# Kernel optimization log

Hardware: AMD Instinct MI355X
Metric: run time of the kernel (lower is better)

## Reference

```python
import jax, jax.numpy as jnp
import numpy as np

N = 8192
IN_DIM = 512
MEM_DIM = 512


def _linear_params(k, fan_in, fan_out):
    kw, kb = jax.random.split(k)
    s = 1.0 / np.sqrt(fan_in)
    W = jax.random.uniform(kw, (fan_in, fan_out), jnp.float32, -s, s)
    b = jax.random.uniform(kb, (fan_out,), jnp.float32, -s, s)
    return W, b


def setup_inputs() -> dict:
    key = jax.random.key(0)
    ks = jax.random.split(key, 12)
    inputs = jax.random.normal(ks[0], (N, IN_DIM), jnp.float32)
    # tree.type is a [1,2] mixing matrix per node (lang vs vis weights)
    type_mask = jax.nn.softmax(jax.random.normal(ks[1], (N, 2), jnp.float32), axis=-1)
    # topologically ordered tree: parent slot of node i is in [0, i]; slot 0 = virtual zero root state
    rng = np.random.default_rng(0)
    parent = np.zeros(N, dtype=np.int32)
    for i in range(1, N):
        parent[i] = rng.integers(0, i + 1)
    d = {"inputs": inputs, "type_mask": type_mask, "parent": jnp.asarray(parent)}
    names = ["ioux_vis", "iouh_vis", "fx_vis", "fh_vis",
             "ioux_lang", "iouh_lang", "fx_lang", "fh_lang"]
    fanins = [IN_DIM, MEM_DIM, IN_DIM, MEM_DIM] * 2
    fanouts = [3 * MEM_DIM, 3 * MEM_DIM, MEM_DIM, MEM_DIM] * 2
    for j, nm in enumerate(names):
        W, b = _linear_params(ks[2 + j], fanins[j], fanouts[j])
        d["W_" + nm] = W
        d["b_" + nm] = b
    return d


def reference(inputs, type_mask, parent,
              W_ioux_vis, b_ioux_vis, W_iouh_vis, b_iouh_vis,
              W_fx_vis, b_fx_vis, W_fh_vis, b_fh_vis,
              W_ioux_lang, b_ioux_lang, W_iouh_lang, b_iouh_lang,
              W_fx_lang, b_fx_lang, W_fh_lang, b_fh_lang):
    n_nodes = inputs.shape[0]
    D = W_fh_vis.shape[1]
    # batch the input-dependent projections into big GEMMs (fused across all nodes)
    x_iou_v = inputs @ W_ioux_vis + b_ioux_vis  # [N, 3D]
    x_f_v = inputs @ W_fx_vis + b_fx_vis        # [N, D]
    x_iou_l = inputs @ W_ioux_lang + b_ioux_lang
    x_f_l = inputs @ W_fx_lang + b_fx_lang

    def node(x_iou, x_f, h_p, c_p, W_iouh, b_iouh, W_fh, b_fh):
        iou = x_iou + h_p @ W_iouh + b_iouh  # [3D]
        i, o, u = jnp.split(iou, 3)
        f = jax.nn.sigmoid(x_f + h_p @ W_fh + b_fh)
        c = jax.nn.sigmoid(i) * jnp.tanh(u) + f * c_p
        h = jax.nn.sigmoid(o) * jnp.tanh(c)
        return c, h

    # slot 0 holds the zero state used by root nodes; node i lives at slot i+1
    c0 = jnp.zeros((n_nodes + 1, D), inputs.dtype)
    h0 = jnp.zeros((n_nodes + 1, D), inputs.dtype)

    def step(carry, xs):
        c_all, h_all = carry
        n, p, xiv, xfv, xil, xfl, tm = xs
        h_p = h_all[p]
        c_p = c_all[p]
        c_v, h_v = node(xiv, xfv, h_p, c_p, W_iouh_vis, b_iouh_vis, W_fh_vis, b_fh_vis)
        c_l, h_l = node(xil, xfl, h_p, c_p, W_iouh_lang, b_iouh_lang, W_fh_lang, b_fh_lang)
        # type_mask @ cat([lang, vis]) == tm[0]*lang + tm[1]*vis
        c_n = tm[0] * c_l + tm[1] * c_v
        h_n = tm[0] * h_l + tm[1] * h_v  # dropout is identity in eval
        return (c_all.at[n + 1].set(c_n), h_all.at[n + 1].set(h_n)), None

    idx = jnp.arange(n_nodes)
    (c_all, h_all), _ = jax.lax.scan(
        step, (c0, h0), (idx, parent, x_iou_v, x_f_v, x_iou_l, x_f_l, type_mask))
    return c_all[1:], h_all[1:]
```

## Files before the change

kernel.cpp:

```cpp
#include <hip/hip_runtime.h>
#include <math.h>

typedef unsigned short ushort_t;
typedef unsigned int uint_t;
typedef unsigned long long u64_t;
typedef __attribute__((ext_vector_type(8))) short short8;
typedef __attribute__((ext_vector_type(4))) float f32x4;

#define N_NODES 8192
#define DIM 512
#define KTOT 1024
#define NCOLS 4096
#define BM 128
#define BN 128
#define NTILE (NCOLS / BN)
#define KIT (KTOT / 32)
#define WIMG_USHORTS ((size_t)NTILE * KIT * 4096)
#define MAXLEV_LDS 128

__device__ __forceinline__ float sigm(float x) { return 1.0f / (1.0f + __expf(-x)); }
__device__ __forceinline__ float tanh_fast(float x) {
    float ax = fabsf(x);
    float e = __expf(2.0f * ax);
    float t = 1.0f - 2.0f / (e + 1.0f);
    return copysignf(t, x);
}
__device__ __forceinline__ uint_t packf(float f) {
    uint_t u = __float_as_uint(f);
    uint_t hi = u & 0xffff0000u;
    float r = f - __uint_as_float(hi);
    return hi | (__float_as_uint(r) >> 16);
}
__device__ __forceinline__ float unpackw(uint_t w) {
    return __uint_as_float(w & 0xffff0000u) + __uint_as_float(w << 16);
}
__device__ __forceinline__ uint_t rne16(float f) {
    uint_t u = __float_as_uint(f);
    return (u + 0x7fffu + ((u >> 16) & 1u)) >> 16;
}

__device__ __forceinline__ void fragAB_u32(const uint4 w0, const uint4 w1,
                                           short8& hi8, short8& lo8) {
    union { uint_t w[4]; short8 s; } H, L;
    uint_t u[8] = { w0.x, w0.y, w0.z, w0.w, w1.x, w1.y, w1.z, w1.w };
#pragma unroll
    for (int j = 0; j < 4; ++j) {
        H.w[j] = (u[2 * j + 1] & 0xffff0000u) | (u[2 * j] >> 16);
        L.w[j] = (u[2 * j + 1] << 16) | (u[2 * j] & 0xffffu);
    }
    hi8 = H.s; lo8 = L.s;
}

__device__ __forceinline__ void fragA_f32(const float4 f0, const float4 f1,
                                          short8& hi8, short8& lo8) {
    union { uint_t w[4]; short8 s; } H, L;
    float f[8] = { f0.x, f0.y, f0.z, f0.w, f1.x, f1.y, f1.z, f1.w };
#pragma unroll
    for (int j = 0; j < 4; ++j) {
        float a = f[2 * j], b = f[2 * j + 1];
        uint_t h0 = __float_as_uint(a) & 0xffff0000u;
        uint_t h1 = __float_as_uint(b) & 0xffff0000u;
        float r0 = a - __uint_as_float(h0);
        float r1 = b - __uint_as_float(h1);
        H.w[j] = h1 | (h0 >> 16);
        L.w[j] = (__float_as_uint(r1) & 0xffff0000u) | (__float_as_uint(r0) >> 16);
    }
    hi8 = H.s; lo8 = L.s;
}

__global__ void __launch_bounds__(256) prep_wimg_kernel(
    const float* __restrict__ Wx_iou_v, const float* __restrict__ Wh_iou_v,
    const float* __restrict__ Wx_f_v,   const float* __restrict__ Wh_f_v,
    const float* __restrict__ Wx_iou_l, const float* __restrict__ Wh_iou_l,
    const float* __restrict__ Wx_f_l,   const float* __restrict__ Wh_f_l,
    ushort_t* __restrict__ Wimg)
{
    __shared__ float T[32][132];
    int p = blockIdx.x >> 5, it = blockIdx.x & 31;
    int tid = threadIdx.x;
#pragma unroll
    for (int e = 0; e < 16; ++e) {
        int lin = e * 256 + tid;
        int dloc = lin & 15, kk = (lin >> 4) & 31, q = lin >> 9;
        int d = p * 16 + dloc;
        int qq = q & 3; bool lang = q >= 4;
        int k = it * 32 + kk;
        const float* W; int col, stride;
        if (qq < 3) { col = qq * DIM + d; stride = 3 * DIM;
            W = (k < DIM) ? (lang ? Wx_iou_l : Wx_iou_v) : (lang ? Wh_iou_l : Wh_iou_v); }
        else        { col = d; stride = DIM;
            W = (k < DIM) ? (lang ? Wx_f_l : Wx_f_v) : (lang ? Wh_f_l : Wh_f_v); }
        int kr = (k < DIM) ? k : (k - DIM);
        T[kk][dloc * 8 + q] = W[(size_t)kr * stride + col];
    }
    __syncthreads();
    size_t tilebase = (size_t)blockIdx.x * 4096;
#pragma unroll
    for (int gch = 0; gch < 2; ++gch) {
        int gi = gch * 256 + tid;
        int col = gi >> 2, gd = gi & 3;
        uint_t wds[4];
#pragma unroll
        for (int i = 0; i < 4; ++i) {
            uint_t v0 = rne16(T[gd * 8 + 2 * i][col]);
            uint_t v1 = rne16(T[gd * 8 + 2 * i + 1][col]);
            wds[i] = (v1 << 16) | v0;
        }
        *(uint4*)(Wimg + tilebase + (size_t)gi * 8) = make_uint4(wds[0], wds[1], wds[2], wds[3]);
    }
}

__global__ void prep_bias_kernel(
    const float* __restrict__ bx_iou_v, const float* __restrict__ bh_iou_v,
    const float* __restrict__ bx_f_v,   const float* __restrict__ bh_f_v,
    const float* __restrict__ bx_iou_l, const float* __restrict__ bh_iou_l,
    const float* __restrict__ bx_f_l,   const float* __restrict__ bh_f_l,
    float* __restrict__ bias)
{
    int j = blockIdx.x * blockDim.x + threadIdx.x;
    if (j >= NCOLS) return;
    int d = j >> 3, q = j & 7;
    int qq = q & 3;
    bool lang = (q & 4) != 0;
    const float* bx; const float* bh; int col;
    if (qq < 3) { col = qq * DIM + d; bx = lang ? bx_iou_l : bx_iou_v; bh = lang ? bh_iou_l : bh_iou_v; }
    else        { col = d;            bx = lang ? bx_f_l  : bx_f_v;   bh = lang ? bh_f_l  : bh_f_v; }
    bias[j] = bx[col] + bh[col];
}

__global__ void __launch_bounds__(1024) levels_sort_kernel(
    const int* __restrict__ parent,
    int* __restrict__ order, int* __restrict__ offsets,
    int* __restrict__ counts, int* __restrict__ cursors,
    int* __restrict__ nlev, int* __restrict__ tilestart,
    int* __restrict__ rbStart, int* __restrict__ nodeHrb)
{
    __shared__ int s_level[N_NODES];
    __shared__ int s_assigned;
    __shared__ int s_maxlev;
    int tid = threadIdx.x;
    int pr[8];
#pragma unroll
    for (int ii = 0; ii < 8; ++ii) {
        int i = tid + ii * 1024;
        pr[ii] = parent[i];
        s_level[i] = -1;
    }
    for (int i = tid; i <= N_NODES; i += 1024) counts[i] = 0;
    if (tid == 0) { s_assigned = 0; s_maxlev = 0; }
    __syncthreads();

    for (int pass = 0; pass <= N_NODES; ++pass) {
        int newly = 0;
#pragma unroll
        for (int ii = 0; ii < 8; ++ii) {
            int i = tid + ii * 1024;
            if (s_level[i] < 0) {
                int p = pr[ii];
                if (p == 0) { s_level[i] = 0; newly++; }
                else { int lp = s_level[p - 1]; if (lp >= 0) { s_level[i] = lp + 1; newly++; } }
            }
        }
        if (newly) atomicAdd(&s_assigned, newly);
        __syncthreads();
        int a = s_assigned;
        if (a >= N_NODES) break;
        __syncthreads();
    }

#pragma unroll
    for (int ii = 0; ii < 8; ++ii) {
        int i = tid + ii * 1024;
        int lv = s_level[i];
        atomicAdd(&counts[lv], 1);
        atomicMax(&s_maxlev, lv);
    }
    __syncthreads();
    if (tid == 0) {
        int nl = s_maxlev + 1;
        nlev[0] = nl;
        int off = 0, toff = 0, rb = 0;
        for (int l = 0; l < nl; ++l) {
            offsets[l] = off; cursors[l] = off;
            tilestart[l] = toff; rbStart[l] = rb;
            int mt = (counts[l] + BM - 1) / BM;
            rb += mt;
            toff += mt * NTILE;
            off += counts[l];
        }
        offsets[nl] = off;
        tilestart[nl] = toff;
        rbStart[nl] = rb;
        nlev[1] = toff;
    }
    __syncthreads();
#pragma unroll
    for (int ii = 0; ii < 8; ++ii) {
        int i = tid + ii * 1024;
        int lv = s_level[i];
        int pos = atomicAdd(&cursors[lv], 1);
        order[pos] = i;
        nodeHrb[i] = rbStart[lv] + ((pos - offsets[lv]) >> 7);
    }
}

__global__ void __launch_bounds__(512, 2) tree_fused_kernel(
    const float* __restrict__ inputs, const float* __restrict__ type_mask,
    const ushort_t* __restrict__ Wimg, const float* __restrict__ bias,
    const int* __restrict__ order, const int* __restrict__ offsets,
    const int* __restrict__ nlev, const int* __restrict__ parent,
    const int* __restrict__ rbStart,
    int* __restrict__ colCnt, int* __restrict__ cCnt,
    uint_t* __restrict__ hPack, uint_t* __restrict__ cPack,
    float* __restrict__ out)
{
    float* cOut = out;
    float* hOut = out + (size_t)N_NODES * DIM;

    __shared__ float eps[BM * 132];
    __shared__ int s_node[BM];
    __shared__ int s_par[BM];
    __shared__ float s_tm[BM][2];
    __shared__ int s_rbs[MAXLEV_LDS];
    __shared__ int s_off[MAXLEV_LDS];

    int tid = threadIdx.x;
    int lane = tid & 63, w = tid >> 6;
    int wr = w >> 1, wc = w & 1;
    int l15 = lane & 15, g = lane >> 4;
    int nl = nlev[0];
    int total = nlev[1];

    int nload = nl + 1; if (nload > MAXLEV_LDS) nload = MAXLEV_LDS;
    for (int i = tid; i < nload; i += 512) { s_rbs[i] = rbStart[i]; s_off[i] = offsets[i]; }
    __syncthreads();

    const ushort_t* bLane = Wimg + (size_t)(wc * 64 + l15) * 32 + (size_t)g * 8;

#define LDB(RB, tilebase, itt) { \
    _Pragma("unroll") for (int n_ = 0; n_ < 4; ++n_) \
        RB[n_] = *(const uint4*)(bLane + (size_t)(tilebase + (itt)) * 4096 + n_ * 512); }

#define LDA_H(RA, itrel) { \
    _Pragma("unroll") for (int m_ = 0; m_ < 2; ++m_) { \
        const uint4* p_ = (const uint4*)(aBaseH[m_] + (itrel) * 32 + g * 8); \
        RA[m_][0] = p_[0]; RA[m_][1] = p_[1]; } }

#define LDA_X(RA, itt) { \
    _Pragma("unroll") for (int m_ = 0; m_ < 2; ++m_) { \
        const float4* p_ = (const float4*)(aBaseX[m_] + (itt) * 32 + g * 8); \
        RA[m_][0] = p_[0]; RA[m_][1] = p_[1]; } }

#define COMP_H(RA, RB) { \
    short8 bh_[4]; \
    _Pragma("unroll") for (int n_ = 0; n_ < 4; ++n_) { \
        union { uint4 u; short8 s; } c_; c_.u = RB[n_]; bh_[n_] = c_.s; } \
    _Pragma("unroll") for (int m_ = 0; m_ < 2; ++m_) { \
        short8 ah_, al_; fragAB_u32(RA[m_][0], RA[m_][1], ah_, al_); \
        _Pragma("unroll") for (int n_ = 0; n_ < 4; ++n_) { \
            acc[m_][n_] = __builtin_amdgcn_mfma_f32_16x16x32_bf16(ah_, bh_[n_], acc[m_][n_], 0, 0, 0); \
            acc[m_][n_] = __builtin_amdgcn_mfma_f32_16x16x32_bf16(al_, bh_[n_], acc[m_][n_], 0, 0, 0); } } }

#define COMP_X(RA, RB) { \
    short8 bh_[4]; \
    _Pragma("unroll") for (int n_ = 0; n_ < 4; ++n_) { \
        union { uint4 u; short8 s; } c_; c_.u = RB[n_]; bh_[n_] = c_.s; } \
    _Pragma("unroll") for (int m_ = 0; m_ < 2; ++m_) { \
        short8 ah_, al_; fragA_f32(RA[m_][0], RA[m_][1], ah_, al_); \
        _Pragma("unroll") for (int n_ = 0; n_ < 4; ++n_) { \
            acc[m_][n_] = __builtin_amdgcn_mfma_f32_16x16x32_bf16(ah_, bh_[n_], acc[m_][n_], 0, 0, 0); \
            acc[m_][n_] = __builtin_amdgcn_mfma_f32_16x16x32_bf16(al_, bh_[n_], acc[m_][n_], 0, 0, 0); } } }

#define POLL16(colPrev, nPrev) { \
    int ok_ = 1; \
    if (lane < 32) { \
        int c_ = __hip_atomic_load(&(colPrev)[lane], __ATOMIC_RELAXED, \
                                   __HIP_MEMORY_SCOPE_AGENT); \
        ok_ = (c_ >= (nPrev)) ? 1 : 0; \
    } \
    uint_t cm_ = (uint_t)(__ballot(ok_) & 0xffffffffu); \
    uint_t pr_ = cm_ & (cm_ >> 1); \
    pmask = 0; \
    _Pragma("unroll") for (int p_ = 0; p_ < 16; ++p_) \
        pmask |= ((pr_ >> (2 * p_)) & 1u) << p_; }

#define GATEI(colPrev, nPrev, itq, slp) { \
    if (!(pmask & (1u << (itq)))) { \
        for (;;) { \
            POLL16(colPrev, nPrev); \
            if (pmask & (1u << (itq))) break; \
            __builtin_amdgcn_s_sleep(slp); \
        } \
        asm volatile("" ::: "memory"); \
    } }

    for (int t = blockIdx.x; t < total; t += gridDim.x) {
        int lev = 0;
        while (lev + 1 < nload && s_rbs[lev + 1] * NTILE <= t) ++lev;
        int lt = t - s_rbs[lev] * NTILE;
        int ntile = lt % NTILE;
        int mt = lt / NTILE;
        int start = s_off[lev];
        int cnt = s_off[lev + 1] - start;
        int jc = ntile * BN;
        int r0 = mt * BM;
        int tbx = ntile * KIT;
        int tbh = ntile * KIT + 16;
        int nPrev = (lev > 0) ? (s_rbs[lev] - s_rbs[lev - 1]) : 0;

        if (tid < BM) {
            int r = r0 + tid;
            int node = (r < cnt) ? order[start + r] : -1;
            s_node[tid] = node;
            int p = (node >= 0) ? parent[node] : 0;
            s_par[tid] = p;
            float t0 = 0.f, t1 = 0.f;
            if (node >= 0) { t0 = type_mask[node * 2]; t1 = type_mask[node * 2 + 1]; }
            s_tm[tid][0] = t0; s_tm[tid][1] = t1;
        }
        __syncthreads();

        f32x4 acc[2][4];
#pragma unroll
        for (int m = 0; m < 2; ++m)
#pragma unroll
            for (int n = 0; n < 4; ++n) acc[m][n] = (f32x4)(0.f);

        {
            const float* aBaseX[2];
#pragma unroll
            for (int m = 0; m < 2; ++m) {
                int nd = s_node[wr * 32 + m * 16 + l15];
                aBaseX[m] = inputs + (size_t)(nd < 0 ? 0 : nd) * DIM;
            }
            float4 xa0[2][2], xa1[2][2]; uint4 xb0[4], xb1[4];
            LDA_X(xa0, 0); LDB(xb0, tbx, 0);
            LDA_X(xa1, 1); LDB(xb1, tbx, 1);
#pragma unroll
            for (int ii = 0; ii < 8; ++ii) {
                int e = 2 * ii, o = e + 1;
                __builtin_amdgcn_s_setprio(1);
                COMP_X(xa0, xb0);
                __builtin_amdgcn_s_setprio(0);
                if (e + 2 < 16) { LDA_X(xa0, e + 2); LDB(xb0, tbx, e + 2); }
                __builtin_amdgcn_s_setprio(1);
                COMP_X(xa1, xb1);
                __builtin_amdgcn_s_setprio(0);
                if (o + 2 < 16) { LDA_X(xa1, o + 2); LDB(xb1, tbx, o + 2); }
            }
        }

        if (lev > 0) {
            const int* colPrev = colCnt + (lev - 1) * NTILE;
            const int it0 = ntile >> 1;
            uint_t pmask = 0;

            const uint_t* aBaseH[2];
#pragma unroll
            for (int m = 0; m < 2; ++m) {
                int p = s_par[wr * 32 + m * 16 + l15];
                aBaseH[m] = hPack + (size_t)((p > 0) ? (p - 1) : 0) * DIM;
            }

#define ITQ(s) ((it0 + (s)) & 15)
            uint4 ha[3][2][2]; uint4 hb[2][4];
            GATEI(colPrev, nPrev, ITQ(0), 2);
            LDA_H(ha[0], ITQ(0)); LDB(hb[0], tbh, ITQ(0));
            GATEI(colPrev, nPrev, ITQ(1), 1);
            LDA_H(ha[1], ITQ(1)); LDB(hb[1], tbh, ITQ(1));
            GATEI(colPrev, nPrev, ITQ(2), 1);
            LDA_H(ha[2], ITQ(2));
#pragma unroll
            for (int s = 0; s < 16; ++s) {
                __builtin_amdgcn_s_setprio(1);
                COMP_H(ha[s % 3], hb[s & 1]);
                __builtin_amdgcn_s_setprio(0);
                if (s + 3 < 16) {
                    GATEI(colPrev, nPrev, ITQ(s + 3), 1);
                    LDA_H(ha[s % 3], ITQ(s + 3));
                }
                if (s + 2 < 16) { LDB(hb[s & 1], tbh, ITQ(s + 2)); }
            }
#undef ITQ
        }

        int cntloc = cnt - r0; if (cntloc > BM) cntloc = BM;
        int erow = tid >> 2, qd = tid & 3;
        int dbase = (jc >> 3) + qd * 4;

        if (lev > 0) {
            const int* cPrev = cCnt + (lev - 1) * NTILE;
            while (__hip_atomic_load(&cPrev[ntile], __ATOMIC_RELAXED,
                                     __HIP_MEMORY_SCOPE_AGENT) < nPrev)
                __builtin_amdgcn_s_sleep(1);
            asm volatile("" ::: "memory");
        }
        float CPv[4];
        {
            int p = (erow < cntloc) ? s_par[erow] : 0;
            uint4 cw = make_uint4(0u, 0u, 0u, 0u);
            if (p > 0) cw = *(const uint4*)(cPack + (size_t)(p - 1) * DIM + dbase);
            CPv[0] = unpackw(cw.x); CPv[1] = unpackw(cw.y);
            CPv[2] = unpackw(cw.z); CPv[3] = unpackw(cw.w);
        }

#pragma unroll
        for (int m = 0; m < 2; ++m)
#pragma unroll
            for (int n = 0; n < 4; ++n) {
                int row = wr * 32 + m * 16 + g * 4;
                int c = wc * 64 + n * 16 + l15;
#pragma unroll
                for (int r = 0; r < 4; ++r) eps[(row + r) * 132 + c] = acc[m][n][r];
            }
        __syncthreads();

        float cn4[4], hn4[4];
        int enode = -1;
        if (erow < cntloc) {
            enode = s_node[erow];
            const float* ep = &eps[erow * 132 + qd * 32];
            float tm0 = s_tm[erow][0], tm1 = s_tm[erow][1];
            float cpl[4] = { CPv[0], CPv[1], CPv[2], CPv[3] };
#pragma unroll
            for (int j = 0; j < 4; ++j) {
                float4 v0 = *(const float4*)(ep + j * 8);
                float4 v1 = *(const float4*)(ep + j * 8 + 4);
                int jb = jc + (qd * 4 + j) * 8;
                float4 b0 = *(const float4*)(bias + jb);
                float4 b1 = *(const float4*)(bias + jb + 4);
                float cp = cpl[j];
                float cv = sigm(v0.x + b0.x) * tanh_fast(v0.z + b0.z)
                         + sigm(v0.w + b0.w) * cp;
                float hv = sigm(v0.y + b0.y) * tanh_fast(cv);
                float cl = sigm(v1.x + b1.x) * tanh_fast(v1.z + b1.z)
                         + sigm(v1.w + b1.w) * cp;
                float hl = sigm(v1.y + b1.y) * tanh_fast(cl);
                cn4[j] = tm0 * cl + tm1 * cv;
                hn4[j] = tm0 * hl + tm1 * hv;
            }
            size_t oi = (size_t)enode * DIM + dbase;
            u64_t h01 = (u64_t)packf(hn4[0]) | ((u64_t)packf(hn4[1]) << 32);
            u64_t h23 = (u64_t)packf(hn4[2]) | ((u64_t)packf(hn4[3]) << 32);
            u64_t* hdst = (u64_t*)(hPack + oi);
            __hip_atomic_store(hdst,     h01, __ATOMIC_RELAXED, __HIP_MEMORY_SCOPE_AGENT);
            __hip_atomic_store(hdst + 1, h23, __ATOMIC_RELAXED, __HIP_MEMORY_SCOPE_AGENT);
        }

        __builtin_amdgcn_s_waitcnt(0);
        __syncthreads();
        if (tid == 0)
            __hip_atomic_fetch_add(&colCnt[lev * NTILE + ntile], 1,
                                   __ATOMIC_RELAXED, __HIP_MEMORY_SCOPE_AGENT);

        if (enode >= 0) {
            size_t oi = (size_t)enode * DIM + dbase;
            u64_t c01 = (u64_t)packf(cn4[0]) | ((u64_t)packf(cn4[1]) << 32);
            u64_t c23 = (u64_t)packf(cn4[2]) | ((u64_t)packf(cn4[3]) << 32);
            u64_t* cdst = (u64_t*)(cPack + oi);
            __hip_atomic_store(cdst,     c01, __ATOMIC_RELAXED, __HIP_MEMORY_SCOPE_AGENT);
            __hip_atomic_store(cdst + 1, c23, __ATOMIC_RELAXED, __HIP_MEMORY_SCOPE_AGENT);
            *(float4*)(cOut + oi) = make_float4(cn4[0], cn4[1], cn4[2], cn4[3]);
            *(float4*)(hOut + oi) = make_float4(hn4[0], hn4[1], hn4[2], hn4[3]);
        }
        __builtin_amdgcn_s_waitcnt(0);
        __syncthreads();
        if (tid == 0)
            __hip_atomic_fetch_add(&cCnt[lev * NTILE + ntile], 1,
                                   __ATOMIC_RELAXED, __HIP_MEMORY_SCOPE_AGENT);
        __syncthreads();
    }
#undef LDB
#undef LDA_H
#undef LDA_X
#undef COMP_H
#undef COMP_X
#undef POLL16
#undef GATEI
}

extern "C" void kernel_launch(void* const* d_in, const int* in_sizes, int n_in,
                              void* d_out, int out_size, void* d_ws, size_t ws_size,
                              hipStream_t stream) {
    const float* inputs      = (const float*)d_in[0];
    const float* type_mask   = (const float*)d_in[1];
    const int*   parent      = (const int*)d_in[2];
    const float* W_ioux_vis  = (const float*)d_in[3];
    const float* b_ioux_vis  = (const float*)d_in[4];
    const float* W_iouh_vis  = (const float*)d_in[5];
    const float* b_iouh_vis  = (const float*)d_in[6];
    const float* W_fx_vis    = (const float*)d_in[7];
    const float* b_fx_vis    = (const float*)d_in[8];
    const float* W_fh_vis    = (const float*)d_in[9];
    const float* b_fh_vis    = (const float*)d_in[10];
    const float* W_ioux_lang = (const float*)d_in[11];
    const float* b_ioux_lang = (const float*)d_in[12];
    const float* W_iouh_lang = (const float*)d_in[13];
    const float* b_iouh_lang = (const float*)d_in[14];
    const float* W_fx_lang   = (const float*)d_in[15];
    const float* b_fx_lang   = (const float*)d_in[16];
    const float* W_fh_lang   = (const float*)d_in[17];
    const float* b_fh_lang   = (const float*)d_in[18];

    ushort_t* Wimg = (ushort_t*)d_ws;
    float* bias    = (float*)(Wimg + WIMG_USHORTS);
    int* order     = (int*)(bias + NCOLS);
    int* offsets   = order + N_NODES;
    int* counts    = offsets + (N_NODES + 2);
    int* cursors   = counts + (N_NODES + 2);
    int* nlev      = cursors + (N_NODES + 2);
    int* tilestart = nlev + 8;
    int* rbStart   = tilestart + (N_NODES + 2);
    int* nodeHrb   = rbStart + (N_NODES + 2);
    int* colCnt    = nodeHrb + N_NODES;
    int* cCnt      = colCnt + MAXLEV_LDS * NTILE;
    size_t off2 = (size_t)((char*)(cCnt + MAXLEV_LDS * NTILE) - (char*)d_ws);
    off2 = (off2 + 255) & ~(size_t)255;
    uint_t* hPack = (uint_t*)((char*)d_ws + off2);
    uint_t* cPack = hPack + (size_t)N_NODES * DIM;

    float* out = (float*)d_out;

    hipMemsetAsync((void*)colCnt, 0, 2 * MAXLEV_LDS * NTILE * sizeof(int), stream);

    hipLaunchKernelGGL(prep_wimg_kernel, dim3(NTILE * KIT), dim3(256), 0, stream,
                       W_ioux_vis, W_iouh_vis, W_fx_vis, W_fh_vis,
                       W_ioux_lang, W_iouh_lang, W_fx_lang, W_fh_lang, Wimg);
    hipLaunchKernelGGL(prep_bias_kernel, dim3(NCOLS / 256), dim3(256), 0, stream,
                       b_ioux_vis, b_iouh_vis, b_fx_vis, b_fh_vis,
                       b_ioux_lang, b_iouh_lang, b_fx_lang, b_fh_lang, bias);
    hipLaunchKernelGGL(levels_sort_kernel, dim3(1), dim3(1024), 0, stream,
                       parent, order, offsets, counts, cursors, nlev, tilestart,
                       rbStart, nodeHrb);

    int occ = 0;
    if (hipOccupancyMaxActiveBlocksPerMultiprocessor(&occ, (const void*)tree_fused_kernel, 512, 0) != hipSuccess || occ < 1)
        occ = 1;
    int bpc = occ < 2 ? occ : 2;
    dim3 grid(256 * bpc);

    void* args[] = { (void*)&inputs, (void*)&type_mask, (void*)&Wimg, (void*)&bias,
                     (void*)&order, (void*)&offsets, (void*)&nlev, (void*)&parent,
                     (void*)&rbStart, (void*)&colCnt, (void*)&cCnt,
                     (void*)&hPack, (void*)&cPack, (void*)&out };
    hipLaunchCooperativeKernel((const void*)tree_fused_kernel, grid, dim3(512), args, 0, stream);
}
```

Baseline: 783.7 us.

## Halve row tile to 64 and remap waves to a 2x4 layout

Reduces BM from 128 to 64 rows per tile and rearranges the 8 waves into 2 row groups by 4 column groups, so each wave computes a 32x32 sub-tile instead of 32x64. The aim is more, smaller row blocks per level, giving better load balance and finer-grained dependency progress for this level-parallel tree recurrence. The epilogue is rewritten to match, with each thread handling 2 output dims instead of 4, and the unused nodeHrb bookkeeping is removed. In exchange there is less weight reuse per loaded B fragment and more total tiles, each paying its own synchronisation and polling cost.

```diff
diff --git a/kernel.cpp b/kernel.cpp
--- a/kernel.cpp
+++ b/kernel.cpp
@@ -11,7 +11,7 @@
 #define DIM 512
 #define KTOT 1024
 #define NCOLS 4096
-#define BM 128
+#define BM 64
 #define BN 128
 #define NTILE (NCOLS / BN)
 #define KIT (KTOT / 32)
@@ -133,7 +133,7 @@
     int* __restrict__ order, int* __restrict__ offsets,
     int* __restrict__ counts, int* __restrict__ cursors,
     int* __restrict__ nlev, int* __restrict__ tilestart,
-    int* __restrict__ rbStart, int* __restrict__ nodeHrb)
+    int* __restrict__ rbStart)
 {
     __shared__ int s_level[N_NODES];
     __shared__ int s_assigned;
@@ -197,10 +197,8 @@
 #pragma unroll
     for (int ii = 0; ii < 8; ++ii) {
         int i = tid + ii * 1024;
-        int lv = s_level[i];
-        int pos = atomicAdd(&cursors[lv], 1);
+        int pos = atomicAdd(&cursors[s_level[i]], 1);
         order[pos] = i;
-        nodeHrb[i] = rbStart[lv] + ((pos - offsets[lv]) >> 7);
     }
 }
 
@@ -226,7 +224,7 @@
 
     int tid = threadIdx.x;
     int lane = tid & 63, w = tid >> 6;
-    int wr = w >> 1, wc = w & 1;
+    int wr = w >> 2, wq = w & 3;
     int l15 = lane & 15, g = lane >> 4;
     int nl = nlev[0];
     int total = nlev[1];
@@ -235,10 +233,10 @@
     for (int i = tid; i < nload; i += 512) { s_rbs[i] = rbStart[i]; s_off[i] = offsets[i]; }
     __syncthreads();
 
-    const ushort_t* bLane = Wimg + (size_t)(wc * 64 + l15) * 32 + (size_t)g * 8;
+    const ushort_t* bLane = Wimg + (size_t)(wq * 32 + l15) * 32 + (size_t)g * 8;
 
 #define LDB(RB, tilebase, itt) { \
-    _Pragma("unroll") for (int n_ = 0; n_ < 4; ++n_) \
+    _Pragma("unroll") for (int n_ = 0; n_ < 2; ++n_) \
         RB[n_] = *(const uint4*)(bLane + (size_t)(tilebase + (itt)) * 4096 + n_ * 512); }
 
 #define LDA_H(RA, itrel) { \
@@ -252,22 +250,22 @@
         RA[m_][0] = p_[0]; RA[m_][1] = p_[1]; } }
 
 #define COMP_H(RA, RB) { \
-    short8 bh_[4]; \
-    _Pragma("unroll") for (int n_ = 0; n_ < 4; ++n_) { \
+    short8 bh_[2]; \
+    _Pragma("unroll") for (int n_ = 0; n_ < 2; ++n_) { \
         union { uint4 u; short8 s; } c_; c_.u = RB[n_]; bh_[n_] = c_.s; } \
     _Pragma("unroll") for (int m_ = 0; m_ < 2; ++m_) { \
         short8 ah_, al_; fragAB_u32(RA[m_][0], RA[m_][1], ah_, al_); \
-        _Pragma("unroll") for (int n_ = 0; n_ < 4; ++n_) { \
+        _Pragma("unroll") for (int n_ = 0; n_ < 2; ++n_) { \
             acc[m_][n_] = __builtin_amdgcn_mfma_f32_16x16x32_bf16(ah_, bh_[n_], acc[m_][n_], 0, 0, 0); \
             acc[m_][n_] = __builtin_amdgcn_mfma_f32_16x16x32_bf16(al_, bh_[n_], acc[m_][n_], 0, 0, 0); } } }
 
 #define COMP_X(RA, RB) { \
-    short8 bh_[4]; \
-    _Pragma("unroll") for (int n_ = 0; n_ < 4; ++n_) { \
+    short8 bh_[2]; \
+    _Pragma("unroll") for (int n_ = 0; n_ < 2; ++n_) { \
         union { uint4 u; short8 s; } c_; c_.u = RB[n_]; bh_[n_] = c_.s; } \
     _Pragma("unroll") for (int m_ = 0; m_ < 2; ++m_) { \
         short8 ah_, al_; fragA_f32(RA[m_][0], RA[m_][1], ah_, al_); \
-        _Pragma("unroll") for (int n_ = 0; n_ < 4; ++n_) { \
+        _Pragma("unroll") for (int n_ = 0; n_ < 2; ++n_) { \
             acc[m_][n_] = __builtin_amdgcn_mfma_f32_16x16x32_bf16(ah_, bh_[n_], acc[m_][n_], 0, 0, 0); \
             acc[m_][n_] = __builtin_amdgcn_mfma_f32_16x16x32_bf16(al_, bh_[n_], acc[m_][n_], 0, 0, 0); } } }
 
@@ -320,11 +318,11 @@
         }
         __syncthreads();
 
-        f32x4 acc[2][4];
+        f32x4 acc[2][2];
 #pragma unroll
         for (int m = 0; m < 2; ++m)
 #pragma unroll
-            for (int n = 0; n < 4; ++n) acc[m][n] = (f32x4)(0.f);
+            for (int n = 0; n < 2; ++n) acc[m][n] = (f32x4)(0.f);
 
         {
             const float* aBaseX[2];
@@ -333,7 +331,7 @@
                 int nd = s_node[wr * 32 + m * 16 + l15];
                 aBaseX[m] = inputs + (size_t)(nd < 0 ? 0 : nd) * DIM;
             }
-            float4 xa0[2][2], xa1[2][2]; uint4 xb0[4], xb1[4];
+            float4 xa0[2][2], xa1[2][2]; uint4 xb0[2], xb1[2];
             LDA_X(xa0, 0); LDB(xb0, tbx, 0);
             LDA_X(xa1, 1); LDB(xb1, tbx, 1);
 #pragma unroll
@@ -363,7 +361,7 @@
             }
 
 #define ITQ(s) ((it0 + (s)) & 15)
-            uint4 ha[3][2][2]; uint4 hb[2][4];
+            uint4 ha[3][2][2]; uint4 hb[2][2];
             GATEI(colPrev, nPrev, ITQ(0), 2);
             LDA_H(ha[0], ITQ(0)); LDB(hb[0], tbh, ITQ(0));
             GATEI(colPrev, nPrev, ITQ(1), 1);
@@ -385,8 +383,8 @@
         }
 
         int cntloc = cnt - r0; if (cntloc > BM) cntloc = BM;
-        int erow = tid >> 2, qd = tid & 3;
-        int dbase = (jc >> 3) + qd * 4;
+        int erow = tid >> 3, qd = tid & 7;
+        int dbase = (jc >> 3) + qd * 2;
 
         if (lev > 0) {
             const int* cPrev = cCnt + (lev - 1) * NTILE;
@@ -395,56 +393,52 @@
                 __builtin_amdgcn_s_sleep(1);
             asm volatile("" ::: "memory");
         }
-        float CPv[4];
+        float CPv[2];
         {
             int p = (erow < cntloc) ? s_par[erow] : 0;
-            uint4 cw = make_uint4(0u, 0u, 0u, 0u);
-            if (p > 0) cw = *(const uint4*)(cPack + (size_t)(p - 1) * DIM + dbase);
+            uint2 cw = make_uint2(0u, 0u);
+            if (p > 0) cw = *(const uint2*)(cPack + (size_t)(p - 1) * DIM + dbase);
             CPv[0] = unpackw(cw.x); CPv[1] = unpackw(cw.y);
-            CPv[2] = unpackw(cw.z); CPv[3] = unpackw(cw.w);
         }
 
 #pragma unroll
         for (int m = 0; m < 2; ++m)
 #pragma unroll
-            for (int n = 0; n < 4; ++n) {
+            for (int n = 0; n < 2; ++n) {
                 int row = wr * 32 + m * 16 + g * 4;
-                int c = wc * 64 + n * 16 + l15;
+                int c = wq * 32 + n * 16 + l15;
 #pragma unroll
                 for (int r = 0; r < 4; ++r) eps[(row + r) * 132 + c] = acc[m][n][r];
             }
         __syncthreads();
 
-        float cn4[4], hn4[4];
+        float cn2[2], hn2[2];
         int enode = -1;
         if (erow < cntloc) {
             enode = s_node[erow];
-            const float* ep = &eps[erow * 132 + qd * 32];
+            const float* ep = &eps[erow * 132 + qd * 16];
             float tm0 = s_tm[erow][0], tm1 = s_tm[erow][1];
-            float cpl[4] = { CPv[0], CPv[1], CPv[2], CPv[3] };
-#pragma unroll
-            for (int j = 0; j < 4; ++j) {
+#pragma unroll
+            for (int j = 0; j < 2; ++j) {
                 float4 v0 = *(const float4*)(ep + j * 8);
                 float4 v1 = *(const float4*)(ep + j * 8 + 4);
-                int jb = jc + (qd * 4 + j) * 8;
+                int jb = jc + (qd * 2 + j) * 8;
                 float4 b0 = *(const float4*)(bias + jb);
                 float4 b1 = *(const float4*)(bias + jb + 4);
-                float cp = cpl[j];
+                float cp = CPv[j];
                 float cv = sigm(v0.x + b0.x) * tanh_fast(v0.z + b0.z)
                          + sigm(v0.w + b0.w) * cp;
                 float hv = sigm(v0.y + b0.y) * tanh_fast(cv);
                 float cl = sigm(v1.x + b1.x) * tanh_fast(v1.z + b1.z)
                          + sigm(v1.w + b1.w) * cp;
                 float hl = sigm(v1.y + b1.y) * tanh_fast(cl);
-                cn4[j] = tm0 * cl + tm1 * cv;
-                hn4[j] = tm0 * hl + tm1 * hv;
+                cn2[j] = tm0 * cl + tm1 * cv;
+                hn2[j] = tm0 * hl + tm1 * hv;
             }
             size_t oi = (size_t)enode * DIM + dbase;
-            u64_t h01 = (u64_t)packf(hn4[0]) | ((u64_t)packf(hn4[1]) << 32);
-            u64_t h23 = (u64_t)packf(hn4[2]) | ((u64_t)packf(hn4[3]) << 32);
-            u64_t* hdst = (u64_t*)(hPack + oi);
-            __hip_atomic_store(hdst,     h01, __ATOMIC_RELAXED, __HIP_MEMORY_SCOPE_AGENT);
-            __hip_atomic_store(hdst + 1, h23, __ATOMIC_RELAXED, __HIP_MEMORY_SCOPE_AGENT);
+            u64_t h01 = (u64_t)packf(hn2[0]) | ((u64_t)packf(hn2[1]) << 32);
+            __hip_atomic_store((u64_t*)(hPack + oi), h01,
+                               __ATOMIC_RELAXED, __HIP_MEMORY_SCOPE_AGENT);
         }
 
         __builtin_amdgcn_s_waitcnt(0);
@@ -455,13 +449,11 @@
 
         if (enode >= 0) {
             size_t oi = (size_t)enode * DIM + dbase;
-            u64_t c01 = (u64_t)packf(cn4[0]) | ((u64_t)packf(cn4[1]) << 32);
-            u64_t c23 = (u64_t)packf(cn4[2]) | ((u64_t)packf(cn4[3]) << 32);
-            u64_t* cdst = (u64_t*)(cPack + oi);
-            __hip_atomic_store(cdst,     c01, __ATOMIC_RELAXED, __HIP_MEMORY_SCOPE_AGENT);
-            __hip_atomic_store(cdst + 1, c23, __ATOMIC_RELAXED, __HIP_MEMORY_SCOPE_AGENT);
-            *(float4*)(cOut + oi) = make_float4(cn4[0], cn4[1], cn4[2], cn4[3]);
-            *(float4*)(hOut + oi) = make_float4(hn4[0], hn4[1], hn4[2], hn4[3]);
+            u64_t c01 = (u64_t)packf(cn2[0]) | ((u64_t)packf(cn2[1]) << 32);
+            __hip_atomic_store((u64_t*)(cPack + oi), c01,
+                               __ATOMIC_RELAXED, __HIP_MEMORY_SCOPE_AGENT);
+            *(float2*)(cOut + oi) = make_float2(cn2[0], cn2[1]);
+            *(float2*)(hOut + oi) = make_float2(hn2[0], hn2[1]);
         }
         __builtin_amdgcn_s_waitcnt(0);
         __syncthreads();
@@ -511,8 +503,7 @@
     int* nlev      = cursors + (N_NODES + 2);
     int* tilestart = nlev + 8;
     int* rbStart   = tilestart + (N_NODES + 2);
-    int* nodeHrb   = rbStart + (N_NODES + 2);
-    int* colCnt    = nodeHrb + N_NODES;
+    int* colCnt    = rbStart + (N_NODES + 2);
     int* cCnt      = colCnt + MAXLEV_LDS * NTILE;
     size_t off2 = (size_t)((char*)(cCnt + MAXLEV_LDS * NTILE) - (char*)d_ws);
     off2 = (off2 + 255) & ~(size_t)255;
@@ -531,7 +522,7 @@
                        b_ioux_lang, b_iouh_lang, b_fx_lang, b_fh_lang, bias);
     hipLaunchKernelGGL(levels_sort_kernel, dim3(1), dim3(1024), 0, stream,
                        parent, order, offsets, counts, cursors, nlev, tilestart,
-                       rbStart, nodeHrb);
+                       rbStart);
 
     int occ = 0;
     if (hipOccupancyMaxActiveBlocksPerMultiprocessor(&occ, (const void*)tree_fused_kernel, 512, 0) != hipSuccess || occ < 1)
```

Measured after the change: 999.3 us. 1.27x slower.
